# Optimization experiments

Measured on AMD Instinct MI355X. Metric: run time of the kernel, lower is better.

## Reference

```python
import jax, jax.numpy as jnp
import numpy as np

B, S, H, STEPS = 4096, 169, 64, 24  # batch, input seq (window 168 + covariate row), hidden, rollout steps


def _lstm(xseq, Wih, Whh, bih, bhh, h0, c0):
    """PyTorch-style single-layer LSTM. xseq: [B,T,D] -> ([B,T,H], hT, cT). Gate order i,f,g,o."""
    xg = jnp.einsum('btd,gd->btg', xseq, Wih) + (bih + bhh)  # precompute input proj [B,T,4H]

    def step(carry, xg_t):
        h, c = carry
        g = xg_t + h @ Whh.T
        i, f, gg, o = jnp.split(g, 4, axis=-1)
        c = jax.nn.sigmoid(f) * c + jax.nn.sigmoid(i) * jnp.tanh(gg)
        h = jax.nn.sigmoid(o) * jnp.tanh(c)
        return (h, c), h

    (hT, cT), hs = jax.lax.scan(step, (h0, c0), jnp.swapaxes(xg, 0, 1))
    return jnp.swapaxes(hs, 0, 1), hT, cT


def reference(x, Wih1, Whh1, bih1, bhh1, Wih2, Whh2, bih2, bhh2, fc1_w, fc1_b, fc2_w, fc2_b):
    win, d = x[:, :-1, :], x[:, -1, :]  # [B,168,1], [B,1]
    z = jnp.zeros((x.shape[0], H), x.dtype)

    def outer(win, _):
        h1s, h1, c1 = _lstm(win, Wih1, Whh1, bih1, bhh1, z, z)
        h1s = jax.nn.relu(h1s)
        # lstm2 is seeded with lstm1's final (h, c) state, as in the torch code
        h2s, _, _ = _lstm(h1s, Wih2, Whh2, bih2, bhh2, h1, c1)
        feat = jnp.concatenate([jax.nn.relu(h2s[:, -1, :]), d], axis=1)  # [B,65]
        out = (feat @ fc1_w.T + fc1_b) @ fc2_w.T + fc2_b  # [B,1] (no relu between fc1/fc2)
        win = jnp.concatenate([win[:, 1:, :], out[:, :, None]], axis=1)  # slide window
        return win, out[:, 0]

    _, outs = jax.lax.scan(outer, win, None, length=STEPS)  # outs: [24,B]
    return jnp.swapaxes(outs, 0, 1)  # [B,24]


def setup_inputs() -> dict:
    key = jax.random.key(0)
    ks = jax.random.split(key, 14)
    bnd = 1.0 / np.sqrt(H)

    def u(k, shape):
        return jax.random.uniform(k, shape, jnp.float32, -bnd, bnd)

    return {
        'x': jax.random.normal(ks[0], (B, S, 1), jnp.float32),
        'Wih1': u(ks[1], (4 * H, 1)),
        'Whh1': u(ks[2], (4 * H, H)),
        'bih1': u(ks[3], (4 * H,)),
        'bhh1': u(ks[4], (4 * H,)),
        'Wih2': u(ks[5], (4 * H, H)),
        'Whh2': u(ks[6], (4 * H, H)),
        'bih2': u(ks[7], (4 * H,)),
        'bhh2': u(ks[8], (4 * H,)),
        'fc1_w': u(ks[9], (64, 65)),
        'fc1_b': u(ks[10], (64,)),
        'fc2_w': u(ks[11], (1, 64)),
        'fc2_b': u(ks[12], (1,)),
    }
```

## Files before the change

### kernel.cpp

```cpp
#include <hip/hip_runtime.h>
#include <stdint.h>

#define NB 16
#define WIN 168
#define NSTEPS 24
#define NBLK (4096/NB)
#define NT 512

typedef __attribute__((ext_vector_type(8))) short bf16x8;
typedef __attribute__((ext_vector_type(4))) float f32x4;
typedef __attribute__((ext_vector_type(2))) float f32x2;

#if __has_builtin(__builtin_amdgcn_rcpf)
#define RCPF(x) __builtin_amdgcn_rcpf(x)
#else
#define RCPF(x) (1.0f / (x))
#endif
#if __has_builtin(__builtin_amdgcn_exp2f)
#define EXP2F(x) __builtin_amdgcn_exp2f(x)
#else
#define EXP2F(x) __expf((x) * 0.6931471805599453f)
#endif

__device__ __forceinline__ float sigm(float x){
  return RCPF(1.0f + EXP2F(x * -1.4426950408889634f));
}
__device__ __forceinline__ float sigtanh(float a, float b){
  float A = EXP2F(a * -1.4426950408889634f);
  float B = EXP2F(fabsf(b) * -2.8853900817779268f);
  float t = (1.0f - B) * RCPF((1.0f + A) * (1.0f + B));
  return __builtin_copysignf(t, b);
}

__device__ __forceinline__ f32x2 exp2v(f32x2 x){ return (f32x2){EXP2F(x.x), EXP2F(x.y)}; }
__device__ __forceinline__ f32x2 rcpv(f32x2 x){ return (f32x2){RCPF(x.x), RCPF(x.y)}; }
__device__ __forceinline__ f32x2 absv(f32x2 x){ return (f32x2){fabsf(x.x), fabsf(x.y)}; }
__device__ __forceinline__ f32x2 csignv(f32x2 t, f32x2 s){
  return (f32x2){__builtin_copysignf(t.x, s.x), __builtin_copysignf(t.y, s.y)};
}
__device__ __forceinline__ f32x2 sigmv(f32x2 x){
  return rcpv(1.0f + exp2v(x * -1.4426950408889634f));
}
__device__ __forceinline__ f32x2 sigtanhv(f32x2 a, f32x2 b){
  f32x2 A = exp2v(a * -1.4426950408889634f);
  f32x2 B = exp2v(absv(b) * -2.8853900817779268f);
  f32x2 t = (1.0f - B) * rcpv((1.0f + A) * (1.0f + B));
  return csignv(t, b);
}

__device__ __forceinline__ uint32_t bf_rn(float f){
  uint32_t u = __builtin_bit_cast(uint32_t, f);
  return (u + 0x7FFFu + ((u >> 16) & 1u)) >> 16;
}
__device__ __forceinline__ float bf_f(uint32_t s){
  return __builtin_bit_cast(float, s << 16);
}
__device__ __forceinline__ void split_t(float f, uint32_t& hi, uint32_t& lo){
  uint32_t u = __builtin_bit_cast(uint32_t, f);
  hi = u >> 16;
  lo = bf_rn(f - bf_f(hi));
}
__device__ __forceinline__ void split_s(float f, short& hi, short& lo){
  uint32_t h = bf_rn(f);
  hi = (short)h;
  lo = (short)bf_rn(f - bf_f(h));
}
__device__ __forceinline__ uint32_t cvtpk2(float a, float b){
  uint32_t r;
  asm("v_cvt_pk_bf16_f32 %0, %1, %2" : "=v"(r) : "v"(a), "v"(b));
  return r;
}
__device__ __forceinline__ float hi_even(uint32_t p){
  return __builtin_bit_cast(float, p << 16);
}
__device__ __forceinline__ float hi_odd(uint32_t p){
  return __builtin_bit_cast(float, p & 0xFFFF0000u);
}
__device__ __forceinline__ f32x4 mfma16(bf16x8 a, bf16x8 b, f32x4 c){
  return __builtin_amdgcn_mfma_f32_16x16x32_bf16(a, b, c, 0, 0, 0);
}

__device__ __forceinline__ void lstm_epi(const f32x4 acc[4], float c[4], float hn[4]){
  #pragma unroll
  for (int p = 0; p < 2; p++){
    const int r0 = 2*p;
    f32x2 gi = {acc[0][r0], acc[0][r0+1]};
    f32x2 gf = {acc[1][r0], acc[1][r0+1]};
    f32x2 gg = {acc[2][r0], acc[2][r0+1]};
    f32x2 go = {acc[3][r0], acc[3][r0+1]};
    f32x2 cc = {c[r0], c[r0+1]};
    f32x2 cn = __builtin_elementwise_fma(sigmv(gf), cc, sigtanhv(gi, gg));
    f32x2 hh = sigtanhv(go, cn);
    c[r0] = cn.x; c[r0+1] = cn.y;
    hn[r0] = hh.x; hn[r0+1] = hh.y;
  }
}

#define FROW 136
#define FBLK 544
#define FB(buf,hl,kt) ((((buf)*2 + (hl))*2 + (kt)) * FBLK)
#define BUF_INTS (2*FBLK)

__global__ __launch_bounds__(NT, 2) void lstm_fused_kernel(
  const float* __restrict__ x,    const float* __restrict__ Wih1, const float* __restrict__ Whh1,
  const float* __restrict__ bih1, const float* __restrict__ bhh1,
  const float* __restrict__ Wih2, const float* __restrict__ Whh2,
  const float* __restrict__ bih2, const float* __restrict__ bhh2,
  const float* __restrict__ fc1w, const float* __restrict__ fc1b,
  const float* __restrict__ fc2w, const float* __restrict__ fc2b,
  float* __restrict__ out, short* __restrict__ hist)
{
  __shared__ __align__(16) short aS[2*2*2*FBLK];
  __shared__ __align__(16) short bS[2*2*2*FBLK];
  __shared__ float cS[64][16];
  __shared__ float win_s[WIN][NB];
  __shared__ float Hlast[NB][68];
  __shared__ float fc1w_s[64*68];
  __shared__ float dval_s[NB];

  const int tid = threadIdx.x;
  const int wv8 = tid >> 6;
  const int wv  = wv8 & 3;
  const bool isA = (wv8 < 4);
  const int ln  = tid & 63;
  const int q   = ln >> 4;
  const int n   = ln & 15;
  const int bg0 = blockIdx.x * NB;
  const int u0  = 16*wv + 4*q;
  const int kt_  = u0 >> 5;
  const int q2_  = (u0 >> 3) & 3;
  const int jj0_ = u0 & 7;
  const int rdo  = q*FROW + n*8;
  const int wro  = q2_*FROW + n*8 + jj0_;
  const int gwo  = kt_*512 + q2_*128 + n*8 + jj0_;
  const int ro   = q*128 + n*8;
  short* __restrict__ hblk = hist + (size_t)blockIdx.x * WIN * 2048;

  for (int i = tid; i < WIN*NB; i += NT){ int t = i >> 4, b = i & 15; win_s[t][b] = x[(bg0 + b)*169 + t]; }
  for (int i = tid; i < 64*65; i += NT){ int j = i / 65, k = i % 65; fc1w_s[j*68 + k] = fc1w[i]; }
  if (tid < NB) dval_s[tid] = x[(bg0 + tid)*169 + 168];

  const float fc1b_r = fc1b[ln];
  const float fc2w_r = fc2w[ln];
  const float fc2b_r = fc2b[0];

  auto fc_head = [&](int s){
    float o2[2];
    #pragma unroll
    for (int bi = 0; bi < 2; bi++){
      const int b = 2*wv8 + bi;
      float a1 = fc1b_r;
      #pragma unroll
      for (int k4 = 0; k4 < 16; k4++){
        const float* wp = &fc1w_s[ln*68 + k4*4];
        const float* hp = &Hlast[b][k4*4];
        a1 += wp[0]*hp[0] + wp[1]*hp[1] + wp[2]*hp[2] + wp[3]*hp[3];
      }
      a1 += dval_s[b] * fc1w_s[ln*68 + 64];
      float v = a1 * fc2w_r;
      #pragma unroll
      for (int off = 32; off > 0; off >>= 1) v += __shfl_xor(v, off);
      o2[bi] = v + fc2b_r;
    }
    if (ln == 0){
      #pragma unroll
      for (int bi = 0; bi < 2; bi++){
        const int b = 2*wv8 + bi;
        out[(bg0 + b)*24 + s] = o2[bi];
        win_s[s % WIN][b] = o2[bi];
      }
    }
  };

  if (isA){
    bf16x8 A1hi[4][2], A1lo[4][2], Ain1[4];
    f32x4 b1c[4];
    #pragma unroll
    for (int e = 0; e < 4; e++){
      const int ja = 64*e + 16*wv + n;
      #pragma unroll
      for (int kt = 0; kt < 2; kt++){
        const float* pw = Whh1 + ja*64 + kt*32 + q*8;
        #pragma unroll
        for (int jj = 0; jj < 8; jj++){ short h,l; split_s(pw[jj], h, l); A1hi[e][kt][jj] = h; A1lo[e][kt][jj] = l; }
      }
      bf16x8 ain = {0,0,0,0,0,0,0,0};
      if (q == 0){ short wh, wl; split_s(Wih1[ja], wh, wl); ain[0] = wh; ain[1] = wh; ain[2] = wl; }
      Ain1[e] = ain;
      const int jc = 64*e + u0;
      #pragma unroll
      for (int r = 0; r < 4; r++) b1c[e][r] = bih1[jc+r] + bhh1[jc+r];
    }
    float c1[4];

    auto lstm1 = [&](int rb, int wb, int slot, int t, bool first){
      f32x4 acc[4];
      bf16x8 bin = {0,0,0,0,0,0,0,0};
      { float xv = win_s[slot][n];
        uint32_t xp = cvtpk2(xv, xv);
        float rx = xv - hi_even(xp);
        uint32_t xq = cvtpk2(rx, rx);
        if (q == 0){ bin[0] = (short)xp; bin[1] = (short)xq; bin[2] = (short)xp; } }
      if (first){
        #pragma unroll
        for (int e = 0; e < 4; e++) acc[e] = mfma16(Ain1[e], bin, b1c[e]);
      } else {
        bf16x8 Bh0 = *(const bf16x8*)&aS[FB(rb,0,0)+rdo];
        bf16x8 Bl0 = *(const bf16x8*)&aS[FB(rb,1,0)+rdo];
        bf16x8 Bh1 = *(const bf16x8*)&aS[FB(rb,0,1)+rdo];
        bf16x8 Bl1 = *(const bf16x8*)&aS[FB(rb,1,1)+rdo];
        #pragma unroll
        for (int e = 0; e < 4; e++){
          f32x4 a = b1c[e];
          a = mfma16(A1hi[e][0], Bh0, a);
          a = mfma16(A1hi[e][0], Bl0, a);
          a = mfma16(A1lo[e][0], Bh0, a);
          a = mfma16(A1hi[e][1], Bh1, a);
          a = mfma16(A1hi[e][1], Bl1, a);
          a = mfma16(A1lo[e][1], Bh1, a);
          a = mfma16(Ain1[e], bin, a);
          acc[e] = a;
        }
      }
      float hn[4];
      lstm_epi(acc, c1, hn);
      uint32_t p01 = cvtpk2(hn[0], hn[1]);
      uint32_t p23 = cvtpk2(hn[2], hn[3]);
      f32x2 r01 = (f32x2){hn[0], hn[1]} - (f32x2){hi_even(p01), hi_odd(p01)};
      f32x2 r23 = (f32x2){hn[2], hn[3]} - (f32x2){hi_even(p23), hi_odd(p23)};
      uint32_t q01 = cvtpk2(r01.x, r01.y);
      uint32_t q23 = cvtpk2(r23.x, r23.y);
      *(uint2*)&aS[FB(wb,0,kt_)+wro] = make_uint2(p01, p23);
      *(uint2*)&aS[FB(wb,1,kt_)+wro] = make_uint2(q01, q23);
      uint32_t m01 = (hn[0] > 0.0f ? 0x0000FFFFu : 0u) | (hn[1] > 0.0f ? 0xFFFF0000u : 0u);
      uint32_t m23 = (hn[2] > 0.0f ? 0x0000FFFFu : 0u) | (hn[3] > 0.0f ? 0xFFFF0000u : 0u);
      short* Hp = hblk + (size_t)t * 2048;
      *(uint2*)&Hp[gwo]        = make_uint2(p01 & m01, p23 & m23);
      *(uint2*)&Hp[1024 + gwo] = make_uint2(q01 & m01, q23 & m23);
    };

    #pragma unroll
    for (int r = 0; r < 4; r++) c1[r] = 0.0f;
    __syncthreads();
    lstm1(0, 1, 0, 0, true);
    for (int t = 1; t < WIN-1; t += 2){
      __syncthreads();
      lstm1(1, 0, t, t, false);
      __syncthreads();
      lstm1(0, 1, t+1, t+1, false);
    }
    __syncthreads();
    lstm1(1, 0, WIN-1, WIN-1, false);
    #pragma unroll
    for (int r = 0; r < 4; r++) cS[u0 + r][n] = c1[r];

    for (int sg = 1; sg < NSTEPS; sg++){
      #pragma unroll
      for (int r = 0; r < 4; r++) c1[r] = 0.0f;
      int slot = sg;
      __syncthreads();
      lstm1(0, 1, slot, 0, true);
      slot++;
      for (int t = 1; t < WIN-1; t += 2){
        __syncthreads();
        lstm1(1, 0, slot, t, false);
        slot++; if (slot == WIN) slot = 0;
        __syncthreads();
        lstm1(0, 1, slot, t+1, false);
        slot++; if (slot == WIN) slot = 0;
      }
      __syncthreads();
      __syncthreads();
      fc_head(sg - 1);
      __syncthreads();
      lstm1(1, 0, slot, WIN-1, false);
      #pragma unroll
      for (int r = 0; r < 4; r++) cS[u0 + r][n] = c1[r];
    }

    for (int i = 0; i < WIN + 1; i++) __syncthreads();
    fc_head(NSTEPS - 1);

  } else {
    bf16x8 A2hi[4][4], A2lo[4][4];
    f32x4 b2c[4];
    #pragma unroll
    for (int e = 0; e < 4; e++){
      const int ja = 64*e + 16*wv + n;
      #pragma unroll
      for (int kt = 0; kt < 4; kt++){
        const float* pw = (kt < 2 ? (Wih2 + ja*64 + kt*32) : (Whh2 + ja*64 + (kt-2)*32)) + q*8;
        #pragma unroll
        for (int jj = 0; jj < 8; jj++){ short h,l; split_s(pw[jj], h, l); A2hi[e][kt][jj] = h; A2lo[e][kt][jj] = l; }
      }
      const int jc = 64*e + u0;
      #pragma unroll
      for (int r = 0; r < 4; r++) b2c[e][r] = bih2[jc+r] + bhh2[jc+r];
    }
    float c2[4];
    bf16x8 ch0, cl0, ch1, cl1, nh0, nl0, nh1, nl1;

    auto loadc = [&](int t){
      const short* Hp = hblk + (size_t)t * 2048;
      ch0 = *(const bf16x8*)&Hp[ro];
      cl0 = *(const bf16x8*)&Hp[1024 + ro];
      ch1 = *(const bf16x8*)&Hp[512 + ro];
      cl1 = *(const bf16x8*)&Hp[1536 + ro];
    };
    auto loadn = [&](int t){
      const short* Hp = hblk + (size_t)t * 2048;
      nh0 = *(const bf16x8*)&Hp[ro];
      nl0 = *(const bf16x8*)&Hp[1024 + ro];
      nh1 = *(const bf16x8*)&Hp[512 + ro];
      nl1 = *(const bf16x8*)&Hp[1536 + ro];
    };
    auto shift = [&](){ ch0 = nh0; cl0 = nl0; ch1 = nh1; cl1 = nl1; };

    auto lstm2 = [&](const short* Sr, int rb, short* Sw, int wb, bool last){
      bf16x8 L2h0 = *(const bf16x8*)&Sr[FB(rb,0,0)+rdo];
      bf16x8 L2l0 = *(const bf16x8*)&Sr[FB(rb,1,0)+rdo];
      bf16x8 L2h1 = *(const bf16x8*)&Sr[FB(rb,0,1)+rdo];
      bf16x8 L2l1 = *(const bf16x8*)&Sr[FB(rb,1,1)+rdo];
      f32x4 acc[4];
      #pragma unroll
      for (int e = 0; e < 4; e++){
        f32x4 a = b2c[e];
        a = mfma16(A2hi[e][0], ch0, a);
        a = mfma16(A2hi[e][0], cl0, a);
        a = mfma16(A2lo[e][0], ch0, a);
        a = mfma16(A2hi[e][1], ch1, a);
        a = mfma16(A2hi[e][1], cl1, a);
        a = mfma16(A2lo[e][1], ch1, a);
        a = mfma16(A2hi[e][2], L2h0, a);
        a = mfma16(A2hi[e][2], L2l0, a);
        a = mfma16(A2lo[e][2], L2h0, a);
        a = mfma16(A2hi[e][3], L2h1, a);
        a = mfma16(A2hi[e][3], L2l1, a);
        a = mfma16(A2lo[e][3], L2h1, a);
        acc[e] = a;
      }
      float hn[4];
      lstm_epi(acc, c2, hn);
      if (!last){
        uint32_t p01 = cvtpk2(hn[0], hn[1]);
        uint32_t p23 = cvtpk2(hn[2], hn[3]);
        f32x2 r01 = (f32x2){hn[0], hn[1]} - (f32x2){hi_even(p01), hi_odd(p01)};
        f32x2 r23 = (f32x2){hn[2], hn[3]} - (f32x2){hi_even(p23), hi_odd(p23)};
        *(uint2*)&Sw[FB(wb,0,kt_)+wro] = make_uint2(p01, p23);
        *(uint2*)&Sw[FB(wb,1,kt_)+wro] = make_uint2(cvtpk2(r01.x, r01.y), cvtpk2(r23.x, r23.y));
      } else {
        #pragma unroll
        for (int r = 0; r < 4; r++) Hlast[n][u0 + r] = fmaxf(hn[r], 0.0f);
      }
    };

    for (int i = 0; i < WIN; i++) __syncthreads();

    for (int sg = 1; sg < NSTEPS; sg++){
      loadc(0);
      loadn(1);
      __syncthreads();
      #pragma unroll
      for (int r = 0; r < 4; r++) c2[r] = cS[u0 + r][n];
      lstm2(aS, 0, bS, 1, false);
      shift();
      for (int t = 1; t < WIN-1; t += 2){
        __syncthreads();
        loadn(t + 1);
        lstm2(bS, 1, bS, 0, false);
        shift();
        __syncthreads();
        loadn(t + 2);
        lstm2(bS, 0, bS, 1, false);
        shift();
      }
      __syncthreads();
      lstm2(bS, 1, bS, 0, true);
      __syncthreads();
      fc_head(sg - 1);
      __syncthreads();
    }

    {
      loadc(0);
      loadn(1);
      __syncthreads();
      #pragma unroll
      for (int r = 0; r < 4; r++) c2[r] = cS[u0 + r][n];
      lstm2(aS, 0, bS, 1, false);
      shift();
      for (int t = 1; t < WIN-1; t += 2){
        __syncthreads();
        loadn(t + 1);
        lstm2(bS, 1, bS, 0, false);
        shift();
        __syncthreads();
        loadn(t + 2);
        lstm2(bS, 0, bS, 1, false);
        shift();
      }
      __syncthreads();
      lstm2(bS, 1, bS, 0, true);
      __syncthreads();
      fc_head(NSTEPS - 1);
    }
  }
}

__global__ __launch_bounds__(256, 1) void lstm_fallback_kernel(
  const float* __restrict__ x,    const float* __restrict__ Wih1, const float* __restrict__ Whh1,
  const float* __restrict__ bih1, const float* __restrict__ bhh1,
  const float* __restrict__ Wih2, const float* __restrict__ Whh2,
  const float* __restrict__ bih2, const float* __restrict__ bhh2,
  const float* __restrict__ fc1w, const float* __restrict__ fc1b,
  const float* __restrict__ fc2w, const float* __restrict__ fc2b,
  float* __restrict__ out)
{
  __shared__ __align__(16) short aS[2*2*2*FBLK];
  __shared__ __align__(16) short r1f[2*2*2*FBLK];
  __shared__ __align__(16) short rlf[2*2*2*FBLK];
  __shared__ float win_s[WIN][NB];
  __shared__ float Hlast[NB][68];
  __shared__ float fc1w_s[64*68];
  __shared__ float dval_s[NB];

  const int tid = threadIdx.x;
  const int wv  = tid >> 6;
  const int ln  = tid & 63;
  const int q   = ln >> 4;
  const int n   = ln & 15;
  const int bg0 = blockIdx.x * NB;
  const int u0  = 16*wv + 4*q;
  const int kt_  = u0 >> 5;
  const int q2_  = (u0 >> 3) & 3;
  const int jj0_ = u0 & 7;
  const int rdo  = q*FROW + n*8;
  const int wro  = q2_*FROW + n*8 + jj0_;

  for (int i = tid; i < WIN*NB; i += 256){ int t = i >> 4, b = i & 15; win_s[t][b] = x[(bg0 + b)*169 + t]; }
  for (int i = tid; i < 64*65; i += 256){ int j = i / 65, k = i % 65; fc1w_s[j*68 + k] = fc1w[i]; }
  if (tid < NB) dval_s[tid] = x[(bg0 + tid)*169 + 168];

  const float fc1b_r = fc1b[ln];
  const float fc2w_r = fc2w[ln];
  const float fc2b_r = fc2b[0];

  bf16x8 A1hi[4][2], A1lo[4][2], Ain1[4];
  bf16x8 A2hi[4][4], A2lo[4][4];
  f32x4 b1c[4], b2c[4];
  #pragma unroll
  for (int e = 0; e < 4; e++){
    const int ja = 64*e + 16*wv + n;
    #pragma unroll
    for (int kt = 0; kt < 2; kt++){
      const float* pw = Whh1 + ja*64 + kt*32 + q*8;
      #pragma unroll
      for (int jj = 0; jj < 8; jj++){ short h,l; split_s(pw[jj], h, l); A1hi[e][kt][jj] = h; A1lo[e][kt][jj] = l; }
    }
    #pragma unroll
    for (int kt = 0; kt < 4; kt++){
      const float* pw = (kt < 2 ? (Wih2 + ja*64 + kt*32) : (Whh2 + ja*64 + (kt-2)*32)) + q*8;
      #pragma unroll
      for (int jj = 0; jj < 8; jj++){ short h,l; split_s(pw[jj], h, l); A2hi[e][kt][jj] = h; A2lo[e][kt][jj] = l; }
    }
    bf16x8 ain = {0,0,0,0,0,0,0,0};
    if (q == 0){ short wh, wl; split_s(Wih1[ja], wh, wl); ain[0] = wh; ain[1] = wh; ain[2] = wl; }
    Ain1[e] = ain;
    const int jc = 64*e + u0;
    #pragma unroll
    for (int r = 0; r < 4; r++){
      b1c[e][r] = bih1[jc+r] + bhh1[jc+r];
      b2c[e][r] = bih2[jc+r] + bhh2[jc+r];
    }
  }

  float c1[4], c2[4], c1r[4];

  auto lstm1_step = [&](short* S, float* cst, int rb, int wb, int slot, bool relu_out){
    bf16x8 Bh0 = *(const bf16x8*)&S[FB(rb,0,0)+rdo];
    bf16x8 Bl0 = *(const bf16x8*)&S[FB(rb,1,0)+rdo];
    bf16x8 Bh1 = *(const bf16x8*)&S[FB(rb,0,1)+rdo];
    bf16x8 Bl1 = *(const bf16x8*)&S[FB(rb,1,1)+rdo];
    bf16x8 bin = {0,0,0,0,0,0,0,0};
    { float xv = win_s[slot][n]; uint32_t xh, xl; split_t(xv, xh, xl);
      if (q == 0){ bin[0] = (short)xh; bin[1] = (short)xl; bin[2] = (short)xh; } }
    f32x4 acc[4];
    #pragma unroll
    for (int e = 0; e < 4; e++){
      f32x4 a = b1c[e];
      a = mfma16(A1hi[e][0], Bh0, a);
      a = mfma16(A1hi[e][0], Bl0, a);
      a = mfma16(A1lo[e][0], Bh0, a);
      a = mfma16(A1hi[e][1], Bh1, a);
      a = mfma16(A1hi[e][1], Bl1, a);
      a = mfma16(A1lo[e][1], Bh1, a);
      a = mfma16(Ain1[e], bin, a);
      acc[e] = a;
    }
    float hn[4];
    #pragma unroll
    for (int r = 0; r < 4; r++){
      float cn = __builtin_fmaf(sigm(acc[1][r]), cst[r], sigtanh(acc[0][r], acc[2][r]));
      cst[r] = cn;
      hn[r] = sigtanh(acc[3][r], cn);
    }
    uint32_t ph[4], pl[4];
    #pragma unroll
    for (int r = 0; r < 4; r++) split_t(hn[r], ph[r], pl[r]);
    *(uint2*)&S[FB(wb,0,kt_)+wro] = make_uint2(ph[0] | (ph[1]<<16), ph[2] | (ph[3]<<16));
    *(uint2*)&S[FB(wb,1,kt_)+wro] = make_uint2(pl[0] | (pl[1]<<16), pl[2] | (pl[3]<<16));
    if (relu_out){
      uint32_t sh[4], sl[4];
      #pragma unroll
      for (int r = 0; r < 4; r++){ bool pos = hn[r] > 0.0f; sh[r] = pos ? ph[r] : 0u; sl[r] = pos ? pl[r] : 0u; }
      *(uint2*)&rlf[FB(rb,0,kt_)+wro] = make_uint2(sh[0] | (sh[1]<<16), sh[2] | (sh[3]<<16));
      *(uint2*)&rlf[FB(rb,1,kt_)+wro] = make_uint2(sl[0] | (sl[1]<<16), sl[2] | (sl[3]<<16));
    }
  };

  auto lstm2_core = [&](bf16x8 L1h0, bf16x8 L1l0, bf16x8 L1h1, bf16x8 L1l1,
                        int rbuf, int wbuf, bool last){
    bf16x8 L2h0 = *(const bf16x8*)&aS[FB(rbuf,0,0)+rdo];
    bf16x8 L2l0 = *(const bf16x8*)&aS[FB(rbuf,1,0)+rdo];
    bf16x8 L2h1 = *(const bf16x8*)&aS[FB(rbuf,0,1)+rdo];
    bf16x8 L2l1 = *(const bf16x8*)&aS[FB(rbuf,1,1)+rdo];
    f32x4 acc[4];
    #pragma unroll
    for (int e = 0; e < 4; e++){
      f32x4 a = b2c[e];
      a = mfma16(A2hi[e][0], L1h0, a);
      a = mfma16(A2hi[e][0], L1l0, a);
      a = mfma16(A2lo[e][0], L1h0, a);
      a = mfma16(A2hi[e][1], L1h1, a);
      a = mfma16(A2hi[e][1], L1l1, a);
      a = mfma16(A2lo[e][1], L1h1, a);
      a = mfma16(A2hi[e][2], L2h0, a);
      a = mfma16(A2hi[e][2], L2l0, a);
      a = mfma16(A2lo[e][2], L2h0, a);
      a = mfma16(A2hi[e][3], L2h1, a);
      a = mfma16(A2hi[e][3], L2l1, a);
      a = mfma16(A2lo[e][3], L2h1, a);
      acc[e] = a;
    }
    float hn[4];
    #pragma unroll
    for (int r = 0; r < 4; r++){
      float cn = __builtin_fmaf(sigm(acc[1][r]), c2[r], sigtanh(acc[0][r], acc[2][r]));
      c2[r] = cn;
      hn[r] = sigtanh(acc[3][r], cn);
    }
    if (!last){
      uint32_t ph[4], pl[4];
      #pragma unroll
      for (int r = 0; r < 4; r++) split_t(hn[r], ph[r], pl[r]);
      *(uint2*)&aS[FB(wbuf,0,kt_)+wro] = make_uint2(ph[0] | (ph[1]<<16), ph[2] | (ph[3]<<16));
      *(uint2*)&aS[FB(wbuf,1,kt_)+wro] = make_uint2(pl[0] | (pl[1]<<16), pl[2] | (pl[3]<<16));
    } else {
      #pragma unroll
      for (int r = 0; r < 4; r++) Hlast[n][u0 + r] = fmaxf(hn[r], 0.0f);
    }
  };

  for (int s = 0; s < NSTEPS; s++){
    { int* p = (int*)&aS[0];
      for (int i = tid; i < BUF_INTS; i += 256) p[i] = 0; }
    #pragma unroll
    for (int r = 0; r < 4; r++) c1[r] = 0.0f;
    int slot = s;
    for (int t = 0; t < WIN; t++){
      __syncthreads();
      lstm1_step(aS, c1, t & 1, (t & 1) ^ 1, slot, false);
      slot++; if (slot == WIN) slot = 0;
    }
    #pragma unroll
    for (int r = 0; r < 4; r++){ c2[r] = c1[r]; c1r[r] = 0.0f; }
    { int* p = (int*)&r1f[0];
      for (int i = tid; i < BUF_INTS; i += 256) p[i] = 0; }
    slot = s;
    __syncthreads();
    lstm1_step(r1f, c1r, 0, 1, slot, true);
    slot++;
    for (int i = 1; i < WIN; i++){
      __syncthreads();
      const int rb = i & 1, wb = rb ^ 1;
      lstm1_step(r1f, c1r, rb, wb, slot, true);
      bf16x8 L1h0 = *(const bf16x8*)&rlf[FB(wb,0,0)+rdo];
      bf16x8 L1l0 = *(const bf16x8*)&rlf[FB(wb,1,0)+rdo];
      bf16x8 L1h1 = *(const bf16x8*)&rlf[FB(wb,0,1)+rdo];
      bf16x8 L1l1 = *(const bf16x8*)&rlf[FB(wb,1,1)+rdo];
      lstm2_core(L1h0, L1l0, L1h1, L1l1, wb, rb, false);
      slot++; if (slot == WIN) slot = 0;
    }
    __syncthreads();
    {
      const int rb = (WIN - 1) & 1;
      bf16x8 L1h0 = *(const bf16x8*)&rlf[FB(rb,0,0)+rdo];
      bf16x8 L1l0 = *(const bf16x8*)&rlf[FB(rb,1,0)+rdo];
      bf16x8 L1h1 = *(const bf16x8*)&rlf[FB(rb,0,1)+rdo];
      bf16x8 L1l1 = *(const bf16x8*)&rlf[FB(rb,1,1)+rdo];
      lstm2_core(L1h0, L1l0, L1h1, L1l1, rb, 0, true);
    }
    __syncthreads();
    {
      float o4[4];
      #pragma unroll
      for (int bi = 0; bi < 4; bi++){
        const int b = 4*wv + bi;
        float a1 = fc1b_r;
        #pragma unroll
        for (int k4 = 0; k4 < 16; k4++){
          const float* wp = &fc1w_s[ln*68 + k4*4];
          const float* hp = &Hlast[b][k4*4];
          a1 += wp[0]*hp[0] + wp[1]*hp[1] + wp[2]*hp[2] + wp[3]*hp[3];
        }
        a1 += dval_s[b] * fc1w_s[ln*68 + 64];
        float v = a1 * fc2w_r;
        #pragma unroll
        for (int off = 32; off > 0; off >>= 1) v += __shfl_xor(v, off);
        o4[bi] = v + fc2b_r;
      }
      if (ln == 0){
        #pragma unroll
        for (int bi = 0; bi < 4; bi++){
          const int b = 4*wv + bi;
          out[(bg0 + b)*24 + s] = o4[bi];
          win_s[s % WIN][b] = o4[bi];
        }
      }
    }
  }
}

extern "C" void kernel_launch(void* const* d_in, const int* in_sizes, int n_in,
                              void* d_out, int out_size, void* d_ws, size_t ws_size,
                              hipStream_t stream) {
  (void)in_sizes; (void)n_in; (void)out_size;
  const size_t need = (size_t)NBLK * WIN * 2048 * sizeof(short);
  if (ws_size >= need){
    lstm_fused_kernel<<<dim3(NBLK), dim3(NT), 0, stream>>>(
        (const float*)d_in[0], (const float*)d_in[1], (const float*)d_in[2],
        (const float*)d_in[3], (const float*)d_in[4], (const float*)d_in[5],
        (const float*)d_in[6], (const float*)d_in[7], (const float*)d_in[8],
        (const float*)d_in[9], (const float*)d_in[10], (const float*)d_in[11],
        (const float*)d_in[12], (float*)d_out, (short*)d_ws);
  } else {
    lstm_fallback_kernel<<<dim3(NBLK), dim3(256), 0, stream>>>(
        (const float*)d_in[0], (const float*)d_in[1], (const float*)d_in[2],
        (const float*)d_in[3], (const float*)d_in[4], (const float*)d_in[5],
        (const float*)d_in[6], (const float*)d_in[7], (const float*)d_in[8],
        (const float*)d_in[9], (const float*)d_in[10], (const float*)d_in[11],
        (const float*)d_in[12], (float*)d_out);
  }
}
```

Measured before the change: 4.837 ms.

## Split LSTM layers into producer/consumer block pairs synchronized by global flags

Adds a pipelined kernel where each batch group gets two blocks: one runs LSTM1 and writes its hidden history to a double-buffered global workspace, the other runs LSTM2 plus the FC head. Per-step global flags let LSTM1 for step sg+1 overlap LSTM2 of step sg, stalling only for the final timestep that needs the fed-back output. This doubles the block count and keeps the two serial recurrences running concurrently, at the cost of extra global traffic and spin-wait synchronization. It relies on co-residency of the paired blocks to avoid deadlock and needs a larger workspace, otherwise it falls back to the old kernel.

New measurement: 4.762 ms. About the same (-1.5%).

```diff
diff --git a/kernel.cpp b/kernel.cpp
--- a/kernel.cpp
+++ b/kernel.cpp
@@ -100,6 +100,301 @@
 #define FBLK 544
 #define FB(buf,hl,kt) ((((buf)*2 + (hl))*2 + (kt)) * FBLK)
 #define BUF_INTS (2*FBLK)
+
+__device__ __forceinline__ void flag_set(uint32_t* f){
+  __threadfence();
+  __hip_atomic_store(f, 1u, __ATOMIC_RELEASE, __HIP_MEMORY_SCOPE_AGENT);
+}
+__device__ __forceinline__ void flag_wait(uint32_t* f){
+  while (__hip_atomic_load(f, __ATOMIC_ACQUIRE, __HIP_MEMORY_SCOPE_AGENT) == 0u)
+    __builtin_amdgcn_s_sleep(2);
+}
+
+__global__ void flags_zero_kernel(uint32_t* flags, int n){
+  int i = blockIdx.x*blockDim.x + threadIdx.x;
+  if (i < n) flags[i] = 0u;
+}
+
+__global__ __launch_bounds__(256, 2) void lstm_pipe_kernel(
+  const float* __restrict__ x,    const float* __restrict__ Wih1, const float* __restrict__ Whh1,
+  const float* __restrict__ bih1, const float* __restrict__ bhh1,
+  const float* __restrict__ Wih2, const float* __restrict__ Whh2,
+  const float* __restrict__ bih2, const float* __restrict__ bhh2,
+  const float* __restrict__ fc1w, const float* __restrict__ fc1b,
+  const float* __restrict__ fc2w, const float* __restrict__ fc2b,
+  float* __restrict__ out, short* __restrict__ hist,
+  short* __restrict__ hoff, float* __restrict__ cg, uint32_t* __restrict__ flags)
+{
+  __shared__ __align__(16) short aS[2*2*2*FBLK];
+  __shared__ __align__(16) short bS[2*2*2*FBLK];
+  __shared__ float win_s[WIN][NB];
+  __shared__ float Hlast[NB][68];
+  __shared__ float fc1w_s[64*68];
+  __shared__ float dval_s[NB];
+
+  const int b   = blockIdx.x >> 1;
+  const bool isA = ((blockIdx.x & 1) == 0);
+  const int tid = threadIdx.x;
+  const int wv  = tid >> 6;
+  const int ln  = tid & 63;
+  const int q   = ln >> 4;
+  const int n   = ln & 15;
+  const int bg0 = b * NB;
+  const int u0  = 16*wv + 4*q;
+  const int kt_  = u0 >> 5;
+  const int q2_  = (u0 >> 3) & 3;
+  const int jj0_ = u0 & 7;
+  const int rdo  = q*FROW + n*8;
+  const int wro  = q2_*FROW + n*8 + jj0_;
+  const int gwo  = kt_*512 + q2_*128 + n*8 + jj0_;
+  const int ro   = q*128 + n*8;
+
+  short* __restrict__ hoffb = hoff + (size_t)b * (4*FBLK);
+  float* __restrict__ cgb   = cg + (size_t)b * 1024;
+  uint32_t* flagA  = flags + (size_t)b * 64;
+  uint32_t* flagFC = flags + (size_t)b * 64 + 32;
+  short* hb = nullptr;
+
+  if (isA){
+    for (int i = tid; i < WIN*NB; i += 256){ int t = i >> 4, bb = i & 15; win_s[t][bb] = x[(bg0 + bb)*169 + t]; }
+
+    bf16x8 A1hi[4][2], A1lo[4][2], Ain1[4];
+    f32x4 b1c[4];
+    #pragma unroll
+    for (int e = 0; e < 4; e++){
+      const int ja = 64*e + 16*wv + n;
+      #pragma unroll
+      for (int kt = 0; kt < 2; kt++){
+        const float* pw = Whh1 + ja*64 + kt*32 + q*8;
+        #pragma unroll
+        for (int jj = 0; jj < 8; jj++){ short h,l; split_s(pw[jj], h, l); A1hi[e][kt][jj] = h; A1lo[e][kt][jj] = l; }
+      }
+      bf16x8 ain = {0,0,0,0,0,0,0,0};
+      if (q == 0){ short wh, wl; split_s(Wih1[ja], wh, wl); ain[0] = wh; ain[1] = wh; ain[2] = wl; }
+      Ain1[e] = ain;
+      const int jc = 64*e + u0;
+      #pragma unroll
+      for (int r = 0; r < 4; r++) b1c[e][r] = bih1[jc+r] + bhh1[jc+r];
+    }
+    float c1[4];
+
+    auto lstm1 = [&](int rb, int wb, float xv, int t, bool first, bool fin){
+      f32x4 acc[4];
+      bf16x8 bin = {0,0,0,0,0,0,0,0};
+      { uint32_t xp = cvtpk2(xv, xv);
+        float rx = xv - hi_even(xp);
+        uint32_t xq = cvtpk2(rx, rx);
+        if (q == 0){ bin[0] = (short)xp; bin[1] = (short)xq; bin[2] = (short)xp; } }
+      if (first){
+        #pragma unroll
+        for (int e = 0; e < 4; e++) acc[e] = mfma16(Ain1[e], bin, b1c[e]);
+      } else {
+        bf16x8 Bh0 = *(const bf16x8*)&aS[FB(rb,0,0)+rdo];
+        bf16x8 Bl0 = *(const bf16x8*)&aS[FB(rb,1,0)+rdo];
+        bf16x8 Bh1 = *(const bf16x8*)&aS[FB(rb,0,1)+rdo];
+        bf16x8 Bl1 = *(const bf16x8*)&aS[FB(rb,1,1)+rdo];
+        #pragma unroll
+        for (int e = 0; e < 4; e++){
+          f32x4 a = b1c[e];
+          a = mfma16(A1hi[e][0], Bh0, a);
+          a = mfma16(A1hi[e][0], Bl0, a);
+          a = mfma16(A1lo[e][0], Bh0, a);
+          a = mfma16(A1hi[e][1], Bh1, a);
+          a = mfma16(A1hi[e][1], Bl1, a);
+          a = mfma16(A1lo[e][1], Bh1, a);
+          a = mfma16(Ain1[e], bin, a);
+          acc[e] = a;
+        }
+      }
+      float hn[4];
+      lstm_epi(acc, c1, hn);
+      uint32_t p01 = cvtpk2(hn[0], hn[1]);
+      uint32_t p23 = cvtpk2(hn[2], hn[3]);
+      f32x2 r01 = (f32x2){hn[0], hn[1]} - (f32x2){hi_even(p01), hi_odd(p01)};
+      f32x2 r23 = (f32x2){hn[2], hn[3]} - (f32x2){hi_even(p23), hi_odd(p23)};
+      uint32_t q01 = cvtpk2(r01.x, r01.y);
+      uint32_t q23 = cvtpk2(r23.x, r23.y);
+      *(uint2*)&aS[FB(wb,0,kt_)+wro] = make_uint2(p01, p23);
+      *(uint2*)&aS[FB(wb,1,kt_)+wro] = make_uint2(q01, q23);
+      uint32_t m01 = (hn[0] > 0.0f ? 0x0000FFFFu : 0u) | (hn[1] > 0.0f ? 0xFFFF0000u : 0u);
+      uint32_t m23 = (hn[2] > 0.0f ? 0x0000FFFFu : 0u) | (hn[3] > 0.0f ? 0xFFFF0000u : 0u);
+      short* Hp = hb + (size_t)t * 2048;
+      *(uint2*)&Hp[gwo]        = make_uint2(p01 & m01, p23 & m23);
+      *(uint2*)&Hp[1024 + gwo] = make_uint2(q01 & m01, q23 & m23);
+      if (fin){
+        *(uint2*)&hoffb[FB(0,0,kt_)+wro] = make_uint2(p01, p23);
+        *(uint2*)&hoffb[FB(0,1,kt_)+wro] = make_uint2(q01, q23);
+      }
+    };
+
+    auto getx = [&](int sg, int t)->float{
+      int s = sg + t;
+      if (s < WIN) return win_s[s][n];
+      return out[(bg0 + n)*24 + (s - WIN)];
+    };
+
+    for (int sg = 0; sg < NSTEPS; sg++){
+      hb = hist + ((size_t)((sg & 1)*NBLK + b)) * WIN * 2048;
+      #pragma unroll
+      for (int r = 0; r < 4; r++) c1[r] = 0.0f;
+      __syncthreads();
+      lstm1(0, 1, getx(sg, 0), 0, true, false);
+      for (int t = 1; t < WIN-1; t += 2){
+        __syncthreads();
+        lstm1(1, 0, getx(sg, t), t, false, false);
+        __syncthreads();
+        lstm1(0, 1, getx(sg, t+1), t+1, false, false);
+      }
+      if (sg >= 1){
+        if (tid == 0) flag_wait(&flagFC[sg-1]);
+        __syncthreads();
+        __threadfence();
+      }
+      __syncthreads();
+      lstm1(1, 0, getx(sg, WIN-1), WIN-1, false, true);
+      #pragma unroll
+      for (int r = 0; r < 4; r++) cgb[(u0 + r)*16 + n] = c1[r];
+      __syncthreads();
+      if (tid == 0) flag_set(&flagA[sg]);
+    }
+
+  } else {
+    for (int i = tid; i < 64*65; i += 256){ int j = i / 65, k = i % 65; fc1w_s[j*68 + k] = fc1w[i]; }
+    if (tid < NB) dval_s[tid] = x[(bg0 + tid)*169 + 168];
+
+    const float fc1b_r = fc1b[ln];
+    const float fc2w_r = fc2w[ln];
+    const float fc2b_r = fc2b[0];
+
+    bf16x8 A2hi[4][4], A2lo[4][4];
+    f32x4 b2c[4];
+    #pragma unroll
+    for (int e = 0; e < 4; e++){
+      const int ja = 64*e + 16*wv + n;
+      #pragma unroll
+      for (int kt = 0; kt < 4; kt++){
+        const float* pw = (kt < 2 ? (Wih2 + ja*64 + kt*32) : (Whh2 + ja*64 + (kt-2)*32)) + q*8;
+        #pragma unroll
+        for (int jj = 0; jj < 8; jj++){ short h,l; split_s(pw[jj], h, l); A2hi[e][kt][jj] = h; A2lo[e][kt][jj] = l; }
+      }
+      const int jc = 64*e + u0;
+      #pragma unroll
+      for (int r = 0; r < 4; r++) b2c[e][r] = bih2[jc+r] + bhh2[jc+r];
+    }
+    float c2[4];
+    bf16x8 ch0, cl0, ch1, cl1, nh0, nl0, nh1, nl1;
+
+    auto loadc = [&](int t){
+      const short* Hp = hb + (size_t)t * 2048;
+      ch0 = *(const bf16x8*)&Hp[ro];
+      cl0 = *(const bf16x8*)&Hp[1024 + ro];
+      ch1 = *(const bf16x8*)&Hp[512 + ro];
+      cl1 = *(const bf16x8*)&Hp[1536 + ro];
+    };
+    auto loadn = [&](int t){
+      const short* Hp = hb + (size_t)t * 2048;
+      nh0 = *(const bf16x8*)&Hp[ro];
+      nl0 = *(const bf16x8*)&Hp[1024 + ro];
+      nh1 = *(const bf16x8*)&Hp[512 + ro];
+      nl1 = *(const bf16x8*)&Hp[1536 + ro];
+    };
+    auto shift = [&](){ ch0 = nh0; cl0 = nl0; ch1 = nh1; cl1 = nl1; };
+
+    auto lstm2 = [&](const short* Sr, int rb, short* Sw, int wb, bool last){
+      bf16x8 L2h0 = *(const bf16x8*)&Sr[FB(rb,0,0)+rdo];
+      bf16x8 L2l0 = *(const bf16x8*)&Sr[FB(rb,1,0)+rdo];
+      bf16x8 L2h1 = *(const bf16x8*)&Sr[FB(rb,0,1)+rdo];
+      bf16x8 L2l1 = *(const bf16x8*)&Sr[FB(rb,1,1)+rdo];
+      f32x4 acc[4];
+      #pragma unroll
+      for (int e = 0; e < 4; e++){
+        f32x4 a = b2c[e];
+        a = mfma16(A2hi[e][0], ch0, a);
+        a = mfma16(A2hi[e][0], cl0, a);
+        a = mfma16(A2lo[e][0], ch0, a);
+        a = mfma16(A2hi[e][1], ch1, a);
+        a = mfma16(A2hi[e][1], cl1, a);
+        a = mfma16(A2lo[e][1], ch1, a);
+        a = mfma16(A2hi[e][2], L2h0, a);
+        a = mfma16(A2hi[e][2], L2l0, a);
+        a = mfma16(A2lo[e][2], L2h0, a);
+        a = mfma16(A2hi[e][3], L2h1, a);
+        a = mfma16(A2hi[e][3], L2l1, a);
+        a = mfma16(A2lo[e][3], L2h1, a);
+        acc[e] = a;
+      }
+      float hn[4];
+      lstm_epi(acc, c2, hn);
+      if (!last){
+        uint32_t p01 = cvtpk2(hn[0], hn[1]);
+        uint32_t p23 = cvtpk2(hn[2], hn[3]);
+        f32x2 r01 = (f32x2){hn[0], hn[1]} - (f32x2){hi_even(p01), hi_odd(p01)};
+        f32x2 r23 = (f32x2){hn[2], hn[3]} - (f32x2){hi_even(p23), hi_odd(p23)};
+        *(uint2*)&Sw[FB(wb,0,kt_)+wro] = make_uint2(p01, p23);
+        *(uint2*)&Sw[FB(wb,1,kt_)+wro] = make_uint2(cvtpk2(r01.x, r01.y), cvtpk2(r23.x, r23.y));
+      } else {
+        #pragma unroll
+        for (int r = 0; r < 4; r++) Hlast[n][u0 + r] = fmaxf(hn[r], 0.0f);
+      }
+    };
+
+    auto fc_head = [&](int s){
+      float o4[4];
+      #pragma unroll
+      for (int bi = 0; bi < 4; bi++){
+        const int b4 = 4*wv + bi;
+        float a1 = fc1b_r;
+        #pragma unroll
+        for (int k4 = 0; k4 < 16; k4++){
+          const float* wp = &fc1w_s[ln*68 + k4*4];
+          const float* hp = &Hlast[b4][k4*4];
+          a1 += wp[0]*hp[0] + wp[1]*hp[1] + wp[2]*hp[2] + wp[3]*hp[3];
+        }
+        a1 += dval_s[b4] * fc1w_s[ln*68 + 64];
+        float v = a1 * fc2w_r;
+        #pragma unroll
+        for (int off = 32; off > 0; off >>= 1) v += __shfl_xor(v, off);
+        o4[bi] = v + fc2b_r;
+      }
+      if (ln == 0){
+        #pragma unroll
+        for (int bi = 0; bi < 4; bi++){
+          const int b4 = 4*wv + bi;
+          out[(bg0 + b4)*24 + s] = o4[bi];
+        }
+      }
+    };
+
+    for (int sg = 0; sg < NSTEPS; sg++){
+      if (tid == 0) flag_wait(&flagA[sg]);
+      __syncthreads();
+      __threadfence();
+      hb = hist + ((size_t)((sg & 1)*NBLK + b)) * WIN * 2048;
+      #pragma unroll
+      for (int r = 0; r < 4; r++) c2[r] = cgb[(u0 + r)*16 + n];
+      loadc(0);
+      loadn(1);
+      lstm2(hoffb, 0, bS, 1, false);
+      shift();
+      for (int t = 1; t < WIN-1; t += 2){
+        __syncthreads();
+        loadn(t + 1);
+        lstm2(bS, 1, bS, 0, false);
+        shift();
+        __syncthreads();
+        loadn(t + 2);
+        lstm2(bS, 0, bS, 1, false);
+        shift();
+      }
+      __syncthreads();
+      lstm2(bS, 1, bS, 0, true);
+      __syncthreads();
+      fc_head(sg);
+      __syncthreads();
+      if (tid == 0) flag_set(&flagFC[sg]);
+    }
+  }
+}
 
 __global__ __launch_bounds__(NT, 2) void lstm_fused_kernel(
   const float* __restrict__ x,    const float* __restrict__ Wih1, const float* __restrict__ Whh1,
@@ -635,8 +930,27 @@
                               void* d_out, int out_size, void* d_ws, size_t ws_size,
                               hipStream_t stream) {
   (void)in_sizes; (void)n_in; (void)out_size;
-  const size_t need = (size_t)NBLK * WIN * 2048 * sizeof(short);
-  if (ws_size >= need){
+  const size_t histB = (size_t)2 * NBLK * WIN * 2048 * sizeof(short);
+  const size_t hoffB = (size_t)NBLK * 4 * FBLK * sizeof(short);
+  const size_t cgB   = (size_t)NBLK * 1024 * sizeof(float);
+  const size_t flagB = (size_t)NBLK * 64 * sizeof(uint32_t);
+  const size_t needP = histB + hoffB + cgB + flagB;
+  const size_t needF = (size_t)NBLK * WIN * 2048 * sizeof(short);
+
+  if (ws_size >= needP){
+    short* hist = (short*)d_ws;
+    short* hoff = (short*)((char*)d_ws + histB);
+    float* cg   = (float*)((char*)d_ws + histB + hoffB);
+    uint32_t* flags = (uint32_t*)((char*)d_ws + histB + hoffB + cgB);
+    const int nflags = NBLK * 64;
+    flags_zero_kernel<<<dim3((nflags + 255)/256), dim3(256), 0, stream>>>(flags, nflags);
+    lstm_pipe_kernel<<<dim3(2*NBLK), dim3(256), 0, stream>>>(
+        (const float*)d_in[0], (const float*)d_in[1], (const float*)d_in[2],
+        (const float*)d_in[3], (const float*)d_in[4], (const float*)d_in[5],
+        (const float*)d_in[6], (const float*)d_in[7], (const float*)d_in[8],
+        (const float*)d_in[9], (const float*)d_in[10], (const float*)d_in[11],
+        (const float*)d_in[12], (float*)d_out, hist, hoff, cg, flags);
+  } else if (ws_size >= needF){
     lstm_fused_kernel<<<dim3(NBLK), dim3(NT), 0, stream>>>(
         (const float*)d_in[0], (const float*)d_in[1], (const float*)d_in[2],
         (const float*)d_in[3], (const float*)d_in[4], (const float*)d_in[5],
```
